# Kernel tuning notes

Measured on AMD Instinct MI355X. Metric: run time of the kernel, lower is better.

Reference implementation:

```python
import jax, jax.numpy as jnp
import numpy as np

N = 50000      # nodes
E = 800000     # edges (avg degree 16)
D = 64         # num_hidden
H = 4          # heads
OUT = 64       # out_dim

def setup_inputs() -> dict:
    key = jax.random.key(0)
    k = jax.random.split(key, 5)
    h = jax.random.normal(k[0], (N, D), dtype=jnp.float32)
    edge_index = jax.random.randint(k[1], (2, E), 0, N)
    gate_w = jax.random.normal(k[2], (H, 2 * D), dtype=jnp.float32) * 0.1  # per-head gate Linear weight
    gate_b = jnp.zeros((H,), dtype=jnp.float32)
    W_cat = jax.random.normal(k[3], (OUT, H * D), dtype=jnp.float32) * 0.05
    b_cat = jnp.zeros((OUT,), dtype=jnp.float32)
    return dict(h=h, edge_index=edge_index, gate_w=gate_w, gate_b=gate_b, W_cat=W_cat, b_cat=b_cat)

def reference(h, edge_index, gate_w, gate_b, W_cat, b_cat):
    # eval mode: both dropouts are identity
    row, col = edge_index[0], edge_index[1]
    n, d = h.shape
    # symmetric-ish degree normalization based on out-degree of row (as in original)
    deg = jax.ops.segment_sum(jnp.ones((row.shape[0],), dtype=h.dtype), row, num_segments=n)
    nd = jnp.clip(deg, 1.0) ** -0.5                     # [N]
    hr = h[row]                                          # [E, D] gather (source)
    hc = h[col]                                          # [E, D] gather (target)
    # per-head gate: tanh(Linear(cat(hr, hc))) vectorized over heads
    w1 = gate_w[:, :d]                                   # [H, D]
    w2 = gate_w[:, d:]                                   # [H, D]
    g = jnp.tanh(hr @ w1.T + hc @ w2.T + gate_b)        # [E, H]
    norm = g * (nd[row] * nd[col])[:, None]              # [E, H]
    # message: norm * x_j where x_j = h[source] = hr; aggregate (add) at target = col
    msgs = norm[:, :, None] * hr[:, None, :]             # [E, H, D]
    agg = jax.ops.segment_sum(msgs, col, num_segments=n) # [N, H, D]
    res = agg.reshape(n, -1)                             # concat heads -> [N, H*D]
    return jax.nn.relu(res @ W_cat.T + b_cat)            # [N, OUT]
```

## Files before the change

kernel.cpp:

```cpp
#include <hip/hip_runtime.h>

#define DD 64
#define HH 4
#define OUTC 64
#define CAP 48
#define CHUNK 2048

typedef __attribute__((ext_vector_type(8))) short bf16x8;
typedef __attribute__((ext_vector_type(4))) float f32x4;

__device__ __forceinline__ float fast_tanh(float x) {
    x = fminf(fmaxf(x, -15.f), 15.f);
    float e = __expf(2.f * x);
    return 1.f - 2.f / (e + 1.f);
}

__device__ __forceinline__ unsigned short f2bf(float f) {
    unsigned int u = __float_as_uint(f);
    u = (u + 0x7FFFu + ((u >> 16) & 1u)) >> 16;
    return (unsigned short)u;
}

__global__ __launch_bounds__(256) void partition_kernel(const int* __restrict__ row,
                                                        const int* __restrict__ col,
                                                        unsigned* __restrict__ cbuck,
                                                        unsigned char* __restrict__ rbuck,
                                                        int* __restrict__ ccount,
                                                        int* __restrict__ rcount,
                                                        int E, int NBUK, int BCAP, int nchunks) {
    __shared__ int hist[256];
    __shared__ int scn[256];
    __shared__ int gbase[256];
    __shared__ unsigned stage[CHUNK];
    __shared__ int saddr[CHUNK];
    int tid = threadIdx.x;
    int phaseC = (blockIdx.x < nchunks) ? 1 : 0;
    int chunk = phaseC ? blockIdx.x : blockIdx.x - nchunks;
    int e0 = chunk * CHUNK;
    int n = E - e0;
    if (n > CHUNK) n = CHUNK;
    const int* key = phaseC ? col : row;

    hist[tid] = 0;
    __syncthreads();
    for (int i = tid; i < n; i += 256) atomicAdd(&hist[key[e0 + i] >> 8], 1);
    __syncthreads();
    int v = hist[tid];
    scn[tid] = v;
    __syncthreads();
    for (int d = 1; d < 256; d <<= 1) {
        int a = (tid >= d) ? scn[tid - d] : 0;
        __syncthreads();
        scn[tid] += a;
        __syncthreads();
    }
    int excl = scn[tid] - v;
    scn[tid] = excl;
    if (tid < NBUK && v > 0)
        gbase[tid] = tid * BCAP + atomicAdd(phaseC ? &ccount[tid] : &rcount[tid], v);
    else
        gbase[tid] = tid * BCAP;
    hist[tid] = 0;
    __syncthreads();

    if (phaseC) {
        for (int i = tid; i < n; i += 256) {
            int c = col[e0 + i];
            int r = row[e0 + i];
            int b = c >> 8;
            int k = atomicAdd(&hist[b], 1);
            int p = scn[b] + k;
            stage[p] = ((unsigned)r << 8) | (unsigned)(c & 255);
            saddr[p] = gbase[b] + k;
        }
        __syncthreads();
        for (int i = tid; i < n; i += 256) cbuck[saddr[i]] = stage[i];
    } else {
        unsigned char* stB = (unsigned char*)stage;
        for (int i = tid; i < n; i += 256) {
            int r = row[e0 + i];
            int b = r >> 8;
            int k = atomicAdd(&hist[b], 1);
            int p = scn[b] + k;
            stB[p] = (unsigned char)(r & 255);
            saddr[p] = gbase[b] + k;
        }
        __syncthreads();
        for (int i = tid; i < n; i += 256) rbuck[saddr[i]] = stB[i];
    }
}

#define HSTR 68
__global__ __launch_bounds__(256) void local_prep(const unsigned* __restrict__ cbuck,
                                                  const unsigned char* __restrict__ rbuck,
                                                  const int* __restrict__ ccount,
                                                  const int* __restrict__ rcount,
                                                  int* __restrict__ cnt,
                                                  unsigned short* __restrict__ slots,
                                                  float* __restrict__ nd,
                                                  const float* __restrict__ h,
                                                  const float* __restrict__ gate_w,
                                                  const float* __restrict__ gate_b,
                                                  const float* __restrict__ Wcat,
                                                  float* __restrict__ a12,
                                                  unsigned short* __restrict__ hbs,
                                                  unsigned short* __restrict__ WTbf,
                                                  int N, int NBUK, int BCAP) {
    __shared__ char smem[38400];
    int tid = threadIdx.x;
    int b = blockIdx.x;
    if (b == 3 * NBUK) {
        for (int i = tid; i < 2048; i += 256) {
            int ln = i & 63;
            int ks = (i >> 6) & 7;
            int ct = i >> 9;
            int o = ct * 16 + (ln & 15);
            int kb = ks * 32 + ((ln >> 4) & 3) * 8;
            const float4* src = (const float4*)&Wcat[(size_t)o * 256 + kb];
            float4 w0 = src[0];
            float4 w1 = src[1];
            ushort4* dst = (ushort4*)&WTbf[(size_t)i * 8];
            dst[0] = make_ushort4(f2bf(w0.x), f2bf(w0.y), f2bf(w0.z), f2bf(w0.w));
            dst[1] = make_ushort4(f2bf(w1.x), f2bf(w1.y), f2bf(w1.z), f2bf(w1.w));
        }
        return;
    }
    int* cur = (int*)smem;
    cur[tid] = 0;
    __syncthreads();
    if (b < NBUK) {
        unsigned short* slds = (unsigned short*)(smem + 1024);
        int s = ccount[b];
        if (s > BCAP) s = BCAP;
        const unsigned* src = cbuck + (size_t)b * BCAP;
        int node0 = b << 8;
        for (int i = tid; i < s; i += 256) {
            unsigned rc = src[i];
            int cl = rc & 255;
            int k = atomicAdd(&cur[cl], 1);
            if (k < CAP) slds[cl * CAP + k] = (unsigned short)(rc >> 8);
        }
        __syncthreads();
        int node = node0 + tid;
        if (node < N) cnt[node] = cur[tid];
        uint4* gdst = (uint4*)(slots + (size_t)node0 * CAP);
        const uint4* gsrc = (const uint4*)slds;
        for (int i = tid; i < 1536; i += 256) gdst[i] = gsrc[i];
    } else {
        float* gws = (float*)(smem + 1024);
        float* ndf = (float*)(smem + 3072);
        float* hs = (float*)(smem + 3584);
        int idx = b - NBUK;
        int bb = idx >> 1;
        int half = idx & 1;
        int node0h = (bb << 8) + half * 128;
        int s = rcount[bb];
        if (s > BCAP) s = BCAP;
        const unsigned char* src = rbuck + (size_t)bb * BCAP;
        for (int i = tid; i < s; i += 256) atomicAdd(&cur[src[i]], 1);
        for (int i = tid; i < 512; i += 256) gws[i] = gate_w[i];
        int nn = N - node0h;
        if (nn > 128) nn = 128;
        if (nn < 0) nn = 0;
        int tile4 = nn * 16;
        const float4* hsrc = (const float4*)(h + (size_t)node0h * DD);
        for (int i = tid; i < tile4; i += 256) {
            int j = i >> 4, q = i & 15;
            *(float4*)&hs[j * HSTR + q * 4] = hsrc[i];
        }
        __syncthreads();
        if (tid < nn) {
            int dg = cur[half * 128 + tid];
            float ndv = rsqrtf((float)(dg < 1 ? 1 : dg));
            nd[node0h + tid] = ndv;
            ndf[tid] = ndv;
        }
        __syncthreads();
        int j = tid >> 1, sel = tid & 1;
        if (j < nn) {
            float acc[4];
            acc[0] = acc[1] = acc[2] = acc[3] = 0.f;
            const float4* hrow = (const float4*)&hs[j * HSTR];
#pragma unroll
            for (int q = 0; q < 16; ++q) {
                float4 hv = hrow[q];
#pragma unroll
                for (int m = 0; m < 4; ++m) {
                    float4 gv = *(const float4*)&gws[(sel * 4 + m) * 64 + q * 4];
                    acc[m] += hv.x * gv.x + hv.y * gv.y + hv.z * gv.z + hv.w * gv.w;
                }
            }
            int node = node0h + j;
#pragma unroll
            for (int m = 0; m < 4; ++m) {
                int mm = sel * 4 + m;
                int hd = mm >> 1, part = mm & 1;
                float vv = acc[m] + (part == 0 ? gate_b[hd] : 0.f);
                a12[(size_t)node * 8 + part * 4 + hd] = vv;
            }
        }
        for (int i = tid; i < tile4; i += 256) {
            int j2 = i >> 4, q = i & 15;
            float sc = ndf[j2];
            const float* p = &hs[j2 * HSTR + q * 4];
            ushort4 pv;
            pv.x = f2bf(sc * p[0]);
            pv.y = f2bf(sc * p[1]);
            pv.z = f2bf(sc * p[2]);
            pv.w = f2bf(sc * p[3]);
            *(ushort4*)&hbs[(size_t)(node0h + j2) * DD + q * 4] = pv;
        }
    }
}

__global__ __launch_bounds__(256) void gg_kernel(const int* __restrict__ cnt,
                                                 const unsigned short* __restrict__ slots,
                                                 const float* __restrict__ nd,
                                                 const float* __restrict__ a12,
                                                 const unsigned short* __restrict__ hbs,
                                                 const unsigned short* __restrict__ WTbf,
                                                 const float* __restrict__ b_cat,
                                                 float* __restrict__ out, int N) {
    __shared__ char glds[4 * 6912];
    __shared__ unsigned short A2[16 * 264];
    int tid = threadIdx.x;
    int wv = tid >> 6;
    int lane = tid & 63;
    int quad = lane >> 4;
    int mcol = lane & 15;
    float bb = b_cat[wv * 16 + mcol];

    char* Alds = glds + wv * 6912;
    unsigned short* Au = (unsigned short*)Alds;
    int* rlds = (int*)(Alds + 6144);

    int n0 = blockIdx.x << 4;
    int c0 = n0 + wv * 4;
    int o1, o2, o3, o4;
    {
        int l0 = (c0 + 0 < N) ? cnt[c0 + 0] : 0; if (l0 > CAP) l0 = CAP;
        int l1 = (c0 + 1 < N) ? cnt[c0 + 1] : 0; if (l1 > CAP) l1 = CAP;
        int l2 = (c0 + 2 < N) ? cnt[c0 + 2] : 0; if (l2 > CAP) l2 = CAP;
        int l3 = (c0 + 3 < N) ? cnt[c0 + 3] : 0; if (l3 > CAP) l3 = CAP;
        o1 = l0; o2 = o1 + l1; o3 = o2 + l2; o4 = o3 + l3;
    }
    int K = o4;
    int ksteps = (K + 31) >> 5;
    for (int z = lane; z < ksteps * 256; z += 64) ((unsigned*)Au)[z] = 0u;
    for (int z = lane; z < ksteps * 32; z += 64) rlds[z] = 0;
    for (int p = lane; p < K; p += 64) {
        int i = (p >= o1) + (p >= o2) + (p >= o3);
        int c = c0 + i;
        int off = p - (i == 0 ? 0 : (i == 1 ? o1 : (i == 2 ? o2 : o3)));
        int r = slots[(size_t)c * CAP + off];
        rlds[p] = r;
        float4 a1 = *(const float4*)&a12[(size_t)r * 8];
        float4 a2 = *(const float4*)&a12[(size_t)c * 8 + 4];
        float t0 = fast_tanh(a1.x + a2.x);
        float t1 = fast_tanh(a1.y + a2.y);
        float t2 = fast_tanh(a1.z + a2.z);
        float t3 = fast_tanh(a1.w + a2.w);
        int bidx = (p >> 5) * 512 + ((p >> 3) & 3) * 128 + (p & 7);
        int m0 = i * 4;
        Au[bidx + (m0 + 0) * 8] = f2bf(t0);
        Au[bidx + (m0 + 1) * 8] = f2bf(t1);
        Au[bidx + (m0 + 2) * 8] = f2bf(t2);
        Au[bidx + (m0 + 3) * 8] = f2bf(t3);
    }
    f32x4 acc0 = (f32x4){0.f, 0.f, 0.f, 0.f};
    f32x4 acc1 = (f32x4){0.f, 0.f, 0.f, 0.f};
    f32x4 acc2 = (f32x4){0.f, 0.f, 0.f, 0.f};
    f32x4 acc3 = (f32x4){0.f, 0.f, 0.f, 0.f};
    for (int ks = 0; ks < ksteps; ++ks) {
        bf16x8 af = *(const bf16x8*)(Alds + ks * 1024 + lane * 16);
        int rk[8];
#pragma unroll
        for (int j = 0; j < 8; ++j) rk[j] = rlds[ks * 32 + quad * 8 + j];
#pragma unroll
        for (int nt = 0; nt < 4; ++nt) {
            const unsigned short* hp = hbs + nt * 16 + mcol;
            bf16x8 bf;
#pragma unroll
            for (int j = 0; j < 8; ++j) bf[j] = (short)hp[(size_t)rk[j] << 6];
            if (nt == 0) acc0 = __builtin_amdgcn_mfma_f32_16x16x32_bf16(af, bf, acc0, 0, 0, 0);
            else if (nt == 1) acc1 = __builtin_amdgcn_mfma_f32_16x16x32_bf16(af, bf, acc1, 0, 0, 0);
            else if (nt == 2) acc2 = __builtin_amdgcn_mfma_f32_16x16x32_bf16(af, bf, acc2, 0, 0, 0);
            else acc3 = __builtin_amdgcn_mfma_f32_16x16x32_bf16(af, bf, acc3, 0, 0, 0);
        }
    }
    {
        int node = c0 + quad;
        int nl = wv * 4 + quad;
        float ndv = (node < N) ? nd[node] : 0.f;
        unsigned short* dst = &A2[nl * 264 + mcol];
#pragma unroll
        for (int reg = 0; reg < 4; ++reg) {
            dst[reg * 64 + 0] = f2bf(acc0[reg] * ndv);
            dst[reg * 64 + 16] = f2bf(acc1[reg] * ndv);
            dst[reg * 64 + 32] = f2bf(acc2[reg] * ndv);
            dst[reg * 64 + 48] = f2bf(acc3[reg] * ndv);
        }
    }
    __syncthreads();
    {
        f32x4 c4 = (f32x4){0.f, 0.f, 0.f, 0.f};
#pragma unroll
        for (int ks = 0; ks < 8; ++ks) {
            bf16x8 af = *(const bf16x8*)&A2[mcol * 264 + ks * 32 + quad * 8];
            bf16x8 bf = *(const bf16x8*)&WTbf[(size_t)((wv * 8 + ks) * 64 + lane) * 8];
            c4 = __builtin_amdgcn_mfma_f32_16x16x32_bf16(af, bf, c4, 0, 0, 0);
        }
#pragma unroll
        for (int reg = 0; reg < 4; ++reg) {
            int n = n0 + quad * 4 + reg;
            if (n < N) {
                float v = c4[reg] + bb;
                out[(size_t)n * OUTC + wv * 16 + mcol] = v > 0.f ? v : 0.f;
            }
        }
    }
}

extern "C" void kernel_launch(void* const* d_in, const int* in_sizes, int n_in,
                              void* d_out, int out_size, void* d_ws, size_t ws_size,
                              hipStream_t stream) {
    const float* h      = (const float*)d_in[0];
    const int*   edge   = (const int*)d_in[1];
    const float* gate_w = (const float*)d_in[2];
    const float* gate_b = (const float*)d_in[3];
    const float* Wcat   = (const float*)d_in[4];
    const float* b_cat  = (const float*)d_in[5];
    int N = in_sizes[0] / DD;
    int E = in_sizes[1] / 2;
    const int* row = edge;
    const int* colp = edge + E;
    float* out = (float*)d_out;

    int NBUK = (N + 255) >> 8;
    int BCAP = ((2 * E / NBUK) + 63) & ~63;

    char* ws = (char*)d_ws;
    size_t off = 0;
    size_t pad = ((size_t)NBUK * 4 + 255) & ~255ull;
    int*   ccount = (int*)(ws + off); off += pad;
    int*   rcount = (int*)(ws + off); off += pad;
    int*   cnt    = (int*)(ws + off); off += (size_t)N * 4;
    float* nd     = (float*)(ws + off); off += (size_t)N * 4;
    float* a12    = (float*)(ws + off); off += (size_t)N * 32;
    unsigned short* slots = (unsigned short*)(ws + off);
    off += ((size_t)NBUK * 256 * CAP * 2 + 255) & ~255ull;
    unsigned short* hbs  = (unsigned short*)(ws + off); off += (size_t)N * DD * 2;
    unsigned short* WTbf = (unsigned short*)(ws + off); off += 2048 * 8 * 2;
    char* scratch = ws + off;
    unsigned*      cbuck = (unsigned*)scratch;
    unsigned char* rbuck = (unsigned char*)(scratch + (size_t)NBUK * BCAP * 4);

    hipMemsetAsync(ccount, 0, pad + (size_t)NBUK * 4, stream);

    int nchunks = (E + CHUNK - 1) / CHUNK;
    partition_kernel<<<2 * nchunks, 256, 0, stream>>>(row, colp, cbuck, rbuck, ccount, rcount,
                                                      E, NBUK, BCAP, nchunks);
    local_prep<<<3 * NBUK + 1, 256, 0, stream>>>(cbuck, rbuck, ccount, rcount, cnt, slots, nd,
                                                 h, gate_w, gate_b, Wcat, a12, hbs, WTbf,
                                                 N, NBUK, BCAP);
    int ntiles = (N + 15) >> 4;
    gg_kernel<<<ntiles, 256, 0, stream>>>(cnt, slots, nd, a12, hbs, WTbf, b_cat, out, N);
}
```

Measured before the change: 135.0 us.

## Fuse row and col partition phases into one block with register-cached edges

The partition kernel previously launched separate blocks for the col-keyed and row-keyed bucketing, and each re-read the edge arrays from global memory. Now each block loads its 1024 edges into registers once and runs both bucketing phases back to back. The chunk size is halved so the block count stays about the same. The 256-entry prefix scan now uses wave shuffles plus a small cross-wave sum instead of a barrier-heavy Hillis-Steele loop. The cost is more global atomics per bucket, since there are more chunks, and smaller contiguous scatter runs.

```diff
diff --git a/kernel.cpp b/kernel.cpp
--- a/kernel.cpp
+++ b/kernel.cpp
@@ -4,7 +4,7 @@
 #define HH 4
 #define OUTC 64
 #define CAP 48
-#define CHUNK 2048
+#define CHUNK 1024
 
 typedef __attribute__((ext_vector_type(8))) short bf16x8;
 typedef __attribute__((ext_vector_type(4))) float f32x4;
@@ -27,66 +27,93 @@
                                                         unsigned char* __restrict__ rbuck,
                                                         int* __restrict__ ccount,
                                                         int* __restrict__ rcount,
-                                                        int E, int NBUK, int BCAP, int nchunks) {
+                                                        int E, int NBUK, int BCAP) {
     __shared__ int hist[256];
     __shared__ int scn[256];
     __shared__ int gbase[256];
+    __shared__ int wsum[4];
     __shared__ unsigned stage[CHUNK];
     __shared__ int saddr[CHUNK];
     int tid = threadIdx.x;
-    int phaseC = (blockIdx.x < nchunks) ? 1 : 0;
-    int chunk = phaseC ? blockIdx.x : blockIdx.x - nchunks;
-    int e0 = chunk * CHUNK;
+    int lane = tid & 63;
+    int wv = tid >> 6;
+    int e0 = blockIdx.x * CHUNK;
     int n = E - e0;
     if (n > CHUNK) n = CHUNK;
-    const int* key = phaseC ? col : row;
-
-    hist[tid] = 0;
-    __syncthreads();
-    for (int i = tid; i < n; i += 256) atomicAdd(&hist[key[e0 + i] >> 8], 1);
-    __syncthreads();
-    int v = hist[tid];
-    scn[tid] = v;
-    __syncthreads();
-    for (int d = 1; d < 256; d <<= 1) {
-        int a = (tid >= d) ? scn[tid - d] : 0;
-        __syncthreads();
-        scn[tid] += a;
-        __syncthreads();
-    }
-    int excl = scn[tid] - v;
-    scn[tid] = excl;
-    if (tid < NBUK && v > 0)
-        gbase[tid] = tid * BCAP + atomicAdd(phaseC ? &ccount[tid] : &rcount[tid], v);
-    else
-        gbase[tid] = tid * BCAP;
-    hist[tid] = 0;
-    __syncthreads();
-
-    if (phaseC) {
-        for (int i = tid; i < n; i += 256) {
-            int c = col[e0 + i];
-            int r = row[e0 + i];
-            int b = c >> 8;
-            int k = atomicAdd(&hist[b], 1);
-            int p = scn[b] + k;
-            stage[p] = ((unsigned)r << 8) | (unsigned)(c & 255);
-            saddr[p] = gbase[b] + k;
-        }
-        __syncthreads();
-        for (int i = tid; i < n; i += 256) cbuck[saddr[i]] = stage[i];
-    } else {
-        unsigned char* stB = (unsigned char*)stage;
-        for (int i = tid; i < n; i += 256) {
-            int r = row[e0 + i];
-            int b = r >> 8;
-            int k = atomicAdd(&hist[b], 1);
-            int p = scn[b] + k;
-            stB[p] = (unsigned char)(r & 255);
-            saddr[p] = gbase[b] + k;
-        }
-        __syncthreads();
-        for (int i = tid; i < n; i += 256) rbuck[saddr[i]] = stB[i];
+
+    int r[4], c[4];
+#pragma unroll
+    for (int j = 0; j < 4; ++j) {
+        int i = j * 256 + tid;
+        if (i < n) {
+            r[j] = row[e0 + i];
+            c[j] = col[e0 + i];
+        } else {
+            r[j] = -1;
+            c[j] = -1;
+        }
+    }
+
+#pragma unroll
+    for (int ph = 0; ph < 2; ++ph) {
+        hist[tid] = 0;
+        __syncthreads();
+#pragma unroll
+        for (int j = 0; j < 4; ++j) {
+            int key = ph ? r[j] : c[j];
+            if (key >= 0) atomicAdd(&hist[key >> 8], 1);
+        }
+        __syncthreads();
+        int v = hist[tid];
+        int x = v;
+#pragma unroll
+        for (int d = 1; d < 64; d <<= 1) {
+            int y = __shfl_up(x, d, 64);
+            if (lane >= d) x += y;
+        }
+        if (lane == 63) wsum[wv] = x;
+        __syncthreads();
+        int base = 0;
+#pragma unroll
+        for (int k = 0; k < 4; ++k)
+            if (k < wv) base += wsum[k];
+        scn[tid] = base + x - v;
+        if (tid < NBUK && v > 0)
+            gbase[tid] = tid * BCAP + atomicAdd(ph ? &rcount[tid] : &ccount[tid], v);
+        else
+            gbase[tid] = tid * BCAP;
+        hist[tid] = 0;
+        __syncthreads();
+
+        if (ph == 0) {
+#pragma unroll
+            for (int j = 0; j < 4; ++j) {
+                if (c[j] >= 0) {
+                    int b = c[j] >> 8;
+                    int k = atomicAdd(&hist[b], 1);
+                    int p = scn[b] + k;
+                    stage[p] = ((unsigned)r[j] << 8) | (unsigned)(c[j] & 255);
+                    saddr[p] = gbase[b] + k;
+                }
+            }
+            __syncthreads();
+            for (int i = tid; i < n; i += 256) cbuck[saddr[i]] = stage[i];
+        } else {
+            unsigned char* stB = (unsigned char*)stage;
+#pragma unroll
+            for (int j = 0; j < 4; ++j) {
+                if (r[j] >= 0) {
+                    int b = r[j] >> 8;
+                    int k = atomicAdd(&hist[b], 1);
+                    int p = scn[b] + k;
+                    stB[p] = (unsigned char)(r[j] & 255);
+                    saddr[p] = gbase[b] + k;
+                }
+            }
+            __syncthreads();
+            for (int i = tid; i < n; i += 256) rbuck[saddr[i]] = stB[i];
+        }
+        __syncthreads();
     }
 }
 
@@ -358,8 +385,8 @@
     hipMemsetAsync(ccount, 0, pad + (size_t)NBUK * 4, stream);
 
     int nchunks = (E + CHUNK - 1) / CHUNK;
-    partition_kernel<<<2 * nchunks, 256, 0, stream>>>(row, colp, cbuck, rbuck, ccount, rcount,
-                                                      E, NBUK, BCAP, nchunks);
+    partition_kernel<<<nchunks, 256, 0, stream>>>(row, colp, cbuck, rbuck, ccount, rcount,
+                                                  E, NBUK, BCAP);
     local_prep<<<3 * NBUK + 1, 256, 0, stream>>>(cbuck, rbuck, ccount, rcount, cnt, slots, nd,
                                                  h, gate_w, gate_b, Wcat, a12, hbs, WTbf,
                                                  N, NBUK, BCAP);
```

Result: slower. 149.8 us (+11.0%).
